# Kernel optimization log

Hardware: AMD Instinct MI355X
Metric: run time of the kernel (lower is better)

Reference implementation:

```python
import jax, jax.numpy as jnp
import numpy as np

N = 30000      # nodes
D = 512        # nhid
E = 300000     # edges (before self-loops)
P_FEAT = 0.5   # feature dropout (F.dropout, training=True)
P_ATT = 0.6    # GATConv attention dropout
NEG_SLOPE = 0.2
SCALE = 1.0    # PairNorm scale


def setup_inputs() -> dict:
    key = jax.random.key(0)
    k1, k2, k3, k4, k5, k6 = jax.random.split(key, 6)
    x = jax.random.normal(k1, (N, D), dtype=jnp.float32)
    edge_index = jax.random.randint(k2, (2, E), 0, N, dtype=jnp.int32)
    # GATConv params (heads=1): lin weight, att_src/att_dst vectors, bias
    W = jax.random.normal(k3, (D, D), dtype=jnp.float32) * 0.05
    att_src = jax.random.normal(k4, (D,), dtype=jnp.float32) * 0.05
    att_dst = jax.random.normal(k5, (D,), dtype=jnp.float32) * 0.05
    bias = jax.random.normal(k6, (D,), dtype=jnp.float32) * 0.05
    return {"x": x, "edge_index": edge_index, "W": W,
            "att_src": att_src, "att_dst": att_dst, "bias": bias}


def reference(x, edge_index, W, att_src, att_dst, bias):
    # deterministic dropout masks (module runs with training=True)
    dk = jax.random.key(42)
    k_feat, k_att = jax.random.split(dk)

    # F.dropout(x, 0.5, training=True)
    keep = jax.random.bernoulli(k_feat, 1.0 - P_FEAT, x.shape)
    x = jnp.where(keep, x / (1.0 - P_FEAT), jnp.float32(0.0))

    # GATConv(heads=1): linear transform
    h = x @ W                                     # [N, D]

    # add self-loops (PyG default add_self_loops=True)
    src, dst = edge_index[0], edge_index[1]
    loop = jnp.arange(N, dtype=src.dtype)
    src = jnp.concatenate([src, loop])            # [E+N]
    dst = jnp.concatenate([dst, loop])

    # per-edge attention logits: LeakyReLU(a_src . h_j + a_dst . h_i)
    a_s = h @ att_src                             # [N]
    a_d = h @ att_dst                             # [N]
    e = jax.nn.leaky_relu(a_s[src] + a_d[dst], NEG_SLOPE)   # [E+N]

    # segment softmax over incoming edges of each dst node
    m = jax.ops.segment_max(e, dst, num_segments=N)
    m = jnp.where(jnp.isfinite(m), m, jnp.float32(0.0))
    ee = jnp.exp(e - m[dst])
    s = jax.ops.segment_sum(ee, dst, num_segments=N)
    alpha = ee / (s[dst] + 1e-16)                 # [E+N]

    # attention dropout p=0.6
    keep_a = jax.random.bernoulli(k_att, 1.0 - P_ATT, alpha.shape)
    alpha = jnp.where(keep_a, alpha / (1.0 - P_ATT), jnp.float32(0.0))

    # scatter-aggregate weighted messages, add bias
    out = jax.ops.segment_sum(alpha[:, None] * h[src], dst, num_segments=N) + bias

    # PairNorm 'PN': center columns, scale by mean row norm
    out = out - jnp.mean(out, axis=0)
    rownorm_mean = jnp.sqrt(1e-6 + jnp.mean(jnp.sum(out * out, axis=1)))
    out = SCALE * out / rownorm_mean

    return jax.nn.relu(out)
```

## Files before the change

kernel.cpp:

```cpp
#include <hip/hip_runtime.h>
#include <stdint.h>
#include <math.h>


#define N_NODES 30000
#define MPAD    30080
#define DIM     512
#define NEDGE   300000
#define ETOT    330000
#define AGG_BLOCKS 7500
#define RED_BLOCKS 60
#define RED_ROWS   125

typedef unsigned int u32;
typedef unsigned short u16;

typedef __attribute__((ext_vector_type(8))) short bf16x8;
typedef __attribute__((ext_vector_type(4))) float f32x4;

__host__ __device__ __forceinline__ void threefry2x32(u32 k0, u32 k1, u32 x0, u32 x1,
                                                      u32& o0, u32& o1) {
  u32 ks2 = k0 ^ k1 ^ 0x1BD11BDAu;
#define TF_R(r) { x0 += x1; x1 = (x1 << r) | (x1 >> (32 - r)); x1 ^= x0; }
  x0 += k0; x1 += k1;
  TF_R(13) TF_R(15) TF_R(26) TF_R(6)
  x0 += k1; x1 += ks2 + 1u;
  TF_R(17) TF_R(29) TF_R(16) TF_R(24)
  x0 += ks2; x1 += k0 + 2u;
  TF_R(13) TF_R(15) TF_R(26) TF_R(6)
  x0 += k0; x1 += k1 + 3u;
  TF_R(17) TF_R(29) TF_R(16) TF_R(24)
  x0 += k1; x1 += ks2 + 4u;
  TF_R(13) TF_R(15) TF_R(26) TF_R(6)
  x0 += ks2; x1 += k0 + 5u;
#undef TF_R
  o0 = x0; o1 = x1;
}

__device__ __forceinline__ u32 tf_fold(u32 k0, u32 k1, u32 idx) {
  u32 a, b;
  threefry2x32(k0, k1, 0u, idx, a, b);
  return a ^ b;
}

__device__ __forceinline__ float bf2f(u32 bits16) {
  return __uint_as_float(bits16 << 16);
}
__device__ __forceinline__ u16 f2bf(float f) {
  u32 u = __float_as_uint(f);
  return (u16)((u + 0x7fffu + ((u >> 16) & 1u)) >> 16);
}

__global__ __launch_bounds__(256) void k_cvtW(const float* __restrict__ W,
                                              u16* __restrict__ Wt) {
  __shared__ u16 tile[32][33];
  int b = blockIdx.x;
  int bk = (b & 15) * 32, bn = (b >> 4) * 32;
  int c = threadIdx.x & 31, r = threadIdx.x >> 5;
#pragma unroll
  for (int rr = 0; rr < 32; rr += 8)
    tile[r + rr][c] = f2bf(W[(size_t)(bk + r + rr) * DIM + bn + c]);
  __syncthreads();
#pragma unroll
  for (int rr = 0; rr < 32; rr += 8)
    Wt[(size_t)(bn + r + rr) * DIM + bk + c] = tile[c][r + rr];
}

__global__ __launch_bounds__(256) void k_dropout(const float* __restrict__ x,
                                                 u16* __restrict__ xd,
                                                 u32 kf0, u32 kf1) {
  size_t gid = (size_t)blockIdx.x * 256 + threadIdx.x;
  size_t i0 = gid * 8;
  if (i0 >= (size_t)MPAD * DIM) return;
  uint4 o = make_uint4(0u, 0u, 0u, 0u);
  if (i0 < (size_t)N_NODES * DIM) {
    float4 v0 = *(const float4*)(x + i0);
    float4 v1 = *(const float4*)(x + i0 + 4);
    float xv[8] = {v0.x, v0.y, v0.z, v0.w, v1.x, v1.y, v1.z, v1.w};
    u32 res[4];
#pragma unroll
    for (int p = 0; p < 4; p++) {
      u32 b0 = tf_fold(kf0, kf1, (u32)i0 + 2 * p);
      u32 b1 = tf_fold(kf0, kf1, (u32)i0 + 2 * p + 1);
      u32 r0 = (b0 >> 31) ? 0u : (u32)f2bf(2.0f * xv[2 * p]);
      u32 r1 = (b1 >> 31) ? 0u : (u32)f2bf(2.0f * xv[2 * p + 1]);
      res[p] = r0 | (r1 << 16);
    }
    o = make_uint4(res[0], res[1], res[2], res[3]);
  }
  *(uint4*)(xd + i0) = o;
}

__global__ __launch_bounds__(256) void k_gemm(const u16* __restrict__ A,
                                              const u16* __restrict__ B,
                                              u16* __restrict__ H) {
  __shared__ __align__(16) u16 lA[128 * 32];
  __shared__ __align__(16) u16 lB[128 * 32];
  const int bn = (blockIdx.x & 3) * 128;
  const int bm = (blockIdx.x >> 2) * 128;
  const int tid = threadIdx.x;
  const int wave = tid >> 6, lane = tid & 63;
  const int quad = lane >> 4, l16 = lane & 15;
  const int wrow = (wave & 1) * 64, wcol = (wave >> 1) * 64;

  f32x4 acc[4][4] = {};
  const int srow = tid >> 2;
  const int scq  = (tid & 3) * 8;

  for (int k0 = 0; k0 < DIM; k0 += 32) {
    uint4 va0 = *(const uint4*)(A + (size_t)(bm + srow) * DIM + k0 + scq);
    uint4 va1 = *(const uint4*)(A + (size_t)(bm + 64 + srow) * DIM + k0 + scq);
    uint4 vb0 = *(const uint4*)(B + (size_t)(bn + srow) * DIM + k0 + scq);
    uint4 vb1 = *(const uint4*)(B + (size_t)(bn + 64 + srow) * DIM + k0 + scq);
    __syncthreads();
    *(uint4*)(lA + srow * 32 + scq) = va0;
    *(uint4*)(lA + (64 + srow) * 32 + scq) = va1;
    *(uint4*)(lB + srow * 32 + scq) = vb0;
    *(uint4*)(lB + (64 + srow) * 32 + scq) = vb1;
    __syncthreads();

    bf16x8 af[4], bfr[4];
#pragma unroll
    for (int i = 0; i < 4; i++)
      af[i] = *(const bf16x8*)(lA + (wrow + i * 16 + l16) * 32 + quad * 8);
#pragma unroll
    for (int j = 0; j < 4; j++)
      bfr[j] = *(const bf16x8*)(lB + (wcol + j * 16 + l16) * 32 + quad * 8);
#pragma unroll
    for (int i = 0; i < 4; i++)
#pragma unroll
      for (int j = 0; j < 4; j++)
        acc[i][j] = __builtin_amdgcn_mfma_f32_16x16x32_bf16(af[i], bfr[j], acc[i][j], 0, 0, 0);
  }
#pragma unroll
  for (int i = 0; i < 4; i++) {
#pragma unroll
    for (int r = 0; r < 4; r++) {
      int row = bm + wrow + i * 16 + quad * 4 + r;
      u16* hp = H + (size_t)row * DIM + bn + wcol + l16;
#pragma unroll
      for (int j = 0; j < 4; j++) hp[j * 16] = f2bf(acc[i][j][r]);
    }
  }
}

__global__ __launch_bounds__(256) void k_rowdots(const u16* __restrict__ h,
                                                 const float* __restrict__ atts,
                                                 const float* __restrict__ attd,
                                                 float* __restrict__ a_s,
                                                 float* __restrict__ a_d) {
  int row = blockIdx.x * 4 + (threadIdx.x >> 6);
  if (row >= N_NODES) return;
  int lane = threadIdx.x & 63;
  uint4 hv = *(const uint4*)(h + (size_t)row * DIM + lane * 8);
  float4 s0 = *(const float4*)(atts + lane * 8);
  float4 s1 = *(const float4*)(atts + lane * 8 + 4);
  float4 d0 = *(const float4*)(attd + lane * 8);
  float4 d1 = *(const float4*)(attd + lane * 8 + 4);
  u32 hw[4] = {hv.x, hv.y, hv.z, hv.w};
  float sa[8] = {s0.x, s0.y, s0.z, s0.w, s1.x, s1.y, s1.z, s1.w};
  float da[8] = {d0.x, d0.y, d0.z, d0.w, d1.x, d1.y, d1.z, d1.w};
  float ps = 0.f, pd = 0.f;
#pragma unroll
  for (int p = 0; p < 4; p++) {
    float h0 = bf2f(hw[p] & 0xffffu), h1 = bf2f(hw[p] >> 16);
    ps += h0 * sa[2 * p] + h1 * sa[2 * p + 1];
    pd += h0 * da[2 * p] + h1 * da[2 * p + 1];
  }
#pragma unroll
  for (int d = 1; d < 64; d <<= 1) { ps += __shfl_xor(ps, d); pd += __shfl_xor(pd, d); }
  if (lane == 0) { a_s[row] = ps; a_d[row] = pd; }
}

__global__ __launch_bounds__(256) void k_hist(const int* __restrict__ ei,
                                              int* __restrict__ counts) {
  int i = blockIdx.x * 256 + threadIdx.x;
  if (i >= ETOT) return;
  int d = (i < NEDGE) ? ei[NEDGE + i] : (i - NEDGE);
  atomicAdd(&counts[d], 1);
}

__global__ __launch_bounds__(1024) void k_scan(const int* __restrict__ counts,
                                               int* __restrict__ off,
                                               int* __restrict__ cursor) {
  __shared__ int wsum[16];
  __shared__ int s_total;
  int tid = threadIdx.x, lane = tid & 63, wid = tid >> 6;
  int carry = 0;
  for (int base = 0; base < N_NODES; base += 1024) {
    int i = base + tid;
    int v = (i < N_NODES) ? counts[i] : 0;
    int x = v;
#pragma unroll
    for (int d = 1; d < 64; d <<= 1) {
      int y = __shfl_up(x, d);
      if (lane >= d) x += y;
    }
    if (lane == 63) wsum[wid] = x;
    __syncthreads();
    if (tid == 0) {
      int run = 0;
#pragma unroll
      for (int w = 0; w < 16; w++) { int tv = wsum[w]; wsum[w] = run; run += tv; }
      s_total = run;
    }
    __syncthreads();
    int excl = x - v + wsum[wid] + carry;
    if (i < N_NODES) { off[i] = excl; cursor[i] = excl; }
    carry += s_total;
    __syncthreads();
  }
  if (tid == 0) off[N_NODES] = carry;
}

__global__ __launch_bounds__(256) void k_scatter(const int* __restrict__ ei,
                                                 int* __restrict__ cursor,
                                                 int* __restrict__ perm) {
  int i = blockIdx.x * 256 + threadIdx.x;
  if (i >= ETOT) return;
  int d = (i < NEDGE) ? ei[NEDGE + i] : (i - NEDGE);
  int slot = atomicAdd(&cursor[d], 1);
  perm[slot] = i;
}

__global__ __launch_bounds__(256) void k_aggregate(
    const int* __restrict__ ei, const int* __restrict__ off, const int* __restrict__ perm,
    const float* __restrict__ a_s, const float* __restrict__ a_d,
    const u16* __restrict__ h, const float* __restrict__ bias,
    float* __restrict__ oa, float* __restrict__ colpart,
    float* __restrict__ ssqpart, u32 ka0, u32 ka1) {
  __shared__ float lbuf[4][512];
  int wid = threadIdx.x >> 6;
  int node = blockIdx.x * 4 + wid;
  int lane = threadIdx.x & 63;
  int beg = off[node], end = off[node + 1];
  int deg = end - beg;
  float adn = a_d[node];

  float acc[8] = {0.f, 0.f, 0.f, 0.f, 0.f, 0.f, 0.f, 0.f};

  if (deg <= 64) {
    int idx = beg + lane;
    bool valid = idx < end;
    int s = 0;
    float lg = -3.0e38f;
    u32 keepbits = 0;
    if (valid) {
      int eid = perm[idx];
      s = (eid < NEDGE) ? ei[eid] : (eid - NEDGE);
      lg = a_s[s] + adn;
      lg = (lg < 0.f) ? 0.2f * lg : lg;
      keepbits = tf_fold(ka0, ka1, (u32)eid);
    }
    float mx = lg;
#pragma unroll
    for (int d = 1; d < 64; d <<= 1) mx = fmaxf(mx, __shfl_xor(mx, d));
    float ee = valid ? expf(lg - mx) : 0.f;
    float ssum = ee;
#pragma unroll
    for (int d = 1; d < 64; d <<= 1) ssum += __shfl_xor(ssum, d);
    float inv_s = 2.5f / (ssum + 1e-16f);
    float w = (valid && ((keepbits >> 9) < 3355444u)) ? ee * inv_s : 0.f;

    for (int j = 0; j < deg; j++) {
      float wj = __shfl(w, j);
      if (wj != 0.f) {
        int sj = __shfl(s, j);
        uint4 hv = *(const uint4*)(h + (size_t)sj * DIM + lane * 8);
        u32 hw[4] = {hv.x, hv.y, hv.z, hv.w};
#pragma unroll
        for (int p = 0; p < 4; p++) {
          acc[2 * p]     += wj * bf2f(hw[p] & 0xffffu);
          acc[2 * p + 1] += wj * bf2f(hw[p] >> 16);
        }
      }
    }
  } else {
    float mx = -3.0e38f;
    for (int base = beg; base < end; base += 64) {
      int idx = base + lane;
      if (idx < end) {
        int eid = perm[idx];
        int s = (eid < NEDGE) ? ei[eid] : (eid - NEDGE);
        float lg = a_s[s] + adn;
        lg = (lg < 0.f) ? 0.2f * lg : lg;
        mx = fmaxf(mx, lg);
      }
    }
#pragma unroll
    for (int d = 1; d < 64; d <<= 1) mx = fmaxf(mx, __shfl_xor(mx, d));
    float ssum = 0.f;
    for (int base = beg; base < end; base += 64) {
      int idx = base + lane;
      if (idx < end) {
        int eid = perm[idx];
        int s = (eid < NEDGE) ? ei[eid] : (eid - NEDGE);
        float lg = a_s[s] + adn;
        lg = (lg < 0.f) ? 0.2f * lg : lg;
        ssum += expf(lg - mx);
      }
    }
#pragma unroll
    for (int d = 1; d < 64; d <<= 1) ssum += __shfl_xor(ssum, d);
    float inv_s = 2.5f / (ssum + 1e-16f);
    for (int base = beg; base < end; base += 64) {
      int idx = base + lane;
      float w = 0.f; int s = 0;
      if (idx < end) {
        int eid = perm[idx];
        s = (eid < NEDGE) ? ei[eid] : (eid - NEDGE);
        float lg = a_s[s] + adn;
        lg = (lg < 0.f) ? 0.2f * lg : lg;
        float ee = expf(lg - mx);
        u32 bits = tf_fold(ka0, ka1, (u32)eid);
        if ((bits >> 9) < 3355444u) w = ee * inv_s;
      }
      int cnt = min(64, end - base);
      for (int j = 0; j < cnt; j++) {
        float wj = __shfl(w, j);
        if (wj != 0.f) {
          int sj = __shfl(s, j);
          uint4 hv = *(const uint4*)(h + (size_t)sj * DIM + lane * 8);
          u32 hw[4] = {hv.x, hv.y, hv.z, hv.w};
#pragma unroll
          for (int p = 0; p < 4; p++) {
            acc[2 * p]     += wj * bf2f(hw[p] & 0xffffu);
            acc[2 * p + 1] += wj * bf2f(hw[p] >> 16);
          }
        }
      }
    }
  }

  float4 b0 = *(const float4*)(bias + lane * 8);
  float4 b1 = *(const float4*)(bias + lane * 8 + 4);
  float bb[8] = {b0.x, b0.y, b0.z, b0.w, b1.x, b1.y, b1.z, b1.w};
  float val[8];
#pragma unroll
  for (int t = 0; t < 8; t++) val[t] = acc[t] + bb[t];
  float* op = oa + (size_t)node * DIM + lane * 8;
#pragma unroll
  for (int t = 0; t < 8; t++) op[t] = val[t];
  *(float4*)&lbuf[wid][lane * 8]     = make_float4(val[0], val[1], val[2], val[3]);
  *(float4*)&lbuf[wid][lane * 8 + 4] = make_float4(val[4], val[5], val[6], val[7]);
  __syncthreads();

  int t = threadIdx.x;
  float s0 = 0.f, s1 = 0.f, ssl = 0.f;
#pragma unroll
  for (int w = 0; w < 4; w++) {
    float a = lbuf[w][t], b = lbuf[w][t + 256];
    s0 += a; s1 += b;
    ssl = fmaf(a, a, ssl);
    ssl = fmaf(b, b, ssl);
  }
  colpart[(size_t)blockIdx.x * 512 + t]       = s0;
  colpart[(size_t)blockIdx.x * 512 + 256 + t] = s1;
#pragma unroll
  for (int d = 1; d < 64; d <<= 1) ssl += __shfl_xor(ssl, d);
  __shared__ float wss[4];
  if ((t & 63) == 0) wss[t >> 6] = ssl;
  __syncthreads();
  if (t == 0) ssqpart[blockIdx.x] = wss[0] + wss[1] + wss[2] + wss[3];
}

__global__ __launch_bounds__(256) void k_redstats(const float* __restrict__ colpart,
                                                  const float* __restrict__ ssqpart,
                                                  float* __restrict__ colsum,
                                                  double* __restrict__ ssq) {
  int b = blockIdx.x;
  int t = threadIdx.x;
  int r0 = b * RED_ROWS;
  float s0 = 0.f, s1 = 0.f;
  for (int r = r0; r < r0 + RED_ROWS; r++) {
    s0 += colpart[(size_t)r * 512 + t];
    s1 += colpart[(size_t)r * 512 + 256 + t];
  }
  atomicAdd(&colsum[t], s0);
  atomicAdd(&colsum[t + 256], s1);
  float sl = (t < RED_ROWS) ? ssqpart[r0 + t] : 0.f;
#pragma unroll
  for (int d = 1; d < 64; d <<= 1) sl += __shfl_xor(sl, d);
  __shared__ float w4[4];
  if ((t & 63) == 0) w4[t >> 6] = sl;
  __syncthreads();
  if (t == 0) atomicAdd(ssq, (double)(w4[0] + w4[1] + w4[2] + w4[3]));
}

__global__ __launch_bounds__(512) void k_finalize(const float* __restrict__ colsum,
                                                  const double* __restrict__ ssq,
                                                  float* __restrict__ mu,
                                                  float* __restrict__ invp) {
  __shared__ double sred[8];
  int j = threadIdx.x;
  float m = colsum[j] * (1.0f / 30000.0f);
  mu[j] = m;
  double p = (double)m * (double)m;
#pragma unroll
  for (int d = 1; d < 64; d <<= 1) p += __shfl_xor(p, d);
  int lane = j & 63, wid = j >> 6;
  if (lane == 0) sred[wid] = p;
  __syncthreads();
  if (j == 0) {
    double smu2 = 0.0;
#pragma unroll
    for (int w = 0; w < 8; w++) smu2 += sred[w];
    double centered = ssq[0] - 30000.0 * smu2;
    double mean = centered * (1.0 / 30000.0);
    if (!(mean >= 0.0)) mean = 0.0;
    float rn = sqrtf(1e-6f + (float)mean);
    invp[0] = 1.0f / rn;
  }
}

__global__ __launch_bounds__(256) void k_finalout(const float* __restrict__ oa,
                                                  const float* __restrict__ mu,
                                                  const float* __restrict__ invp,
                                                  float* __restrict__ out) {
  size_t gid = (size_t)blockIdx.x * 256 + threadIdx.x;
  size_t i0 = gid * 4;
  if (i0 >= (size_t)N_NODES * DIM) return;
  float inv = invp[0];
  int j = (int)(i0 & (DIM - 1));
  float4 v = *(const float4*)(oa + i0);
  float4 m = *(const float4*)(mu + j);
  float4 o;
  o.x = (v.x - m.x) * inv; o.x = (o.x < 0.f) ? 0.f : o.x;
  o.y = (v.y - m.y) * inv; o.y = (o.y < 0.f) ? 0.f : o.y;
  o.z = (v.z - m.z) * inv; o.z = (o.z < 0.f) ? 0.f : o.z;
  o.w = (v.w - m.w) * inv; o.w = (o.w < 0.f) ? 0.f : o.w;
  *(float4*)(out + i0) = o;
}

extern "C" void kernel_launch(void* const* d_in, const int* in_sizes, int n_in,
                              void* d_out, int out_size, void* d_ws, size_t ws_size,
                              hipStream_t stream) {
  const float* x    = (const float*)d_in[0];
  const int*   ei   = (const int*)d_in[1];
  const float* W    = (const float*)d_in[2];
  const float* atts = (const float*)d_in[3];
  const float* attd = (const float*)d_in[4];
  const float* bias = (const float*)d_in[5];
  float* out = (float*)d_out;
  char* ws = (char*)d_ws;

  float* oa     = (float*)(ws + 0);
  u16*   xd     = (u16*)(ws + 0);
  u16*   h      = (u16*)(ws + 61440000);
  u16*   Wt     = (u16*)(ws + 92241920);
  float* a_s    = (float*)(ws + 92766208);
  float* a_d    = (float*)(ws + 92886272);
  int*   counts = (int*)(ws + 93006336);
  int*   offs   = (int*)(ws + 93126400);
  int*   cursor = (int*)(ws + 93246464);
  int*   perm   = (int*)(ws + 93366528);
  float* colsum = (float*)(ws + 94686528);
  float* mu     = (float*)(ws + 94688576);
  double* ssq   = (double*)(ws + 94690624);
  float* invp   = (float*)(ws + 94690688);

  float* colpart = out;
  float* ssqpart = out + (size_t)AGG_BLOCKS * 512;

  u32 kf0, kf1, ka0, ka1;
  threefry2x32(0u, 42u, 0u, 0u, kf0, kf1);
  threefry2x32(0u, 42u, 0u, 1u, ka0, ka1);

  hipMemsetAsync(counts, 0, 120064, stream);
  hipMemsetAsync((void*)colsum, 0, 4224, stream);

  k_cvtW<<<256, 256, 0, stream>>>(W, Wt);
  k_dropout<<<7520, 256, 0, stream>>>(x, xd, kf0, kf1);
  k_gemm<<<940, 256, 0, stream>>>(xd, Wt, h);
  k_rowdots<<<7500, 256, 0, stream>>>(h, atts, attd, a_s, a_d);
  k_hist<<<1290, 256, 0, stream>>>(ei, counts);
  k_scan<<<1, 1024, 0, stream>>>(counts, offs, cursor);
  k_scatter<<<1290, 256, 0, stream>>>(ei, cursor, perm);
  k_aggregate<<<AGG_BLOCKS, 256, 0, stream>>>(ei, offs, perm, a_s, a_d, h, bias,
                                              oa, colpart, ssqpart, ka0, ka1);
  k_redstats<<<RED_BLOCKS, 256, 0, stream>>>(colpart, ssqpart, colsum, ssq);
  k_finalize<<<1, 512, 0, stream>>>(colsum, ssq, mu, invp);
  k_finalout<<<15000, 256, 0, stream>>>(oa, mu, invp, out);
}
```

Measured before the change: 304.3 us.

## Fuse attention row-dots into GEMM epilogue and widen K-tile with padded LDS

Removes the separate rowdots kernel. Each GEMM block now reduces its fp32 accumulators against att_src/att_dst and atomically adds per-row partials into a_s/a_d, which are zeroed by a new memset. The GEMM K-step grows from 32 to 64, and LDS rows are padded to 72 elements to reduce bank conflicts and halve the number of barriers. The changes are a launch removed plus a reread of h avoided, in exchange for float atomics (nondeterministic summation order) and dot products computed on unrounded fp32 values instead of bf16 h.

New measurement: 354.8 us. 1.17x slower.

```diff
diff --git a/kernel.cpp b/kernel.cpp
--- a/kernel.cpp
+++ b/kernel.cpp
@@ -11,6 +11,7 @@
 #define AGG_BLOCKS 7500
 #define RED_BLOCKS 60
 #define RED_ROWS   125
+#define LDSW    72
 
 typedef unsigned int u32;
 typedef unsigned short u16;
@@ -93,9 +94,13 @@
 
 __global__ __launch_bounds__(256) void k_gemm(const u16* __restrict__ A,
                                               const u16* __restrict__ B,
-                                              u16* __restrict__ H) {
-  __shared__ __align__(16) u16 lA[128 * 32];
-  __shared__ __align__(16) u16 lB[128 * 32];
+                                              u16* __restrict__ H,
+                                              const float* __restrict__ atts,
+                                              const float* __restrict__ attd,
+                                              float* __restrict__ a_s,
+                                              float* __restrict__ a_d) {
+  __shared__ __align__(16) u16 lA[128 * LDSW];
+  __shared__ __align__(16) u16 lB[128 * LDSW];
   const int bn = (blockIdx.x & 3) * 128;
   const int bm = (blockIdx.x >> 2) * 128;
   const int tid = threadIdx.x;
@@ -104,34 +109,43 @@
   const int wrow = (wave & 1) * 64, wcol = (wave >> 1) * 64;
 
   f32x4 acc[4][4] = {};
-  const int srow = tid >> 2;
-  const int scq  = (tid & 3) * 8;
-
-  for (int k0 = 0; k0 < DIM; k0 += 32) {
-    uint4 va0 = *(const uint4*)(A + (size_t)(bm + srow) * DIM + k0 + scq);
-    uint4 va1 = *(const uint4*)(A + (size_t)(bm + 64 + srow) * DIM + k0 + scq);
-    uint4 vb0 = *(const uint4*)(B + (size_t)(bn + srow) * DIM + k0 + scq);
-    uint4 vb1 = *(const uint4*)(B + (size_t)(bn + 64 + srow) * DIM + k0 + scq);
+
+  for (int k0 = 0; k0 < DIM; k0 += 64) {
+    uint4 ra[4], rb[4];
+#pragma unroll
+    for (int p = 0; p < 4; p++) {
+      int idx = tid + p * 256;
+      int row = idx >> 3, c8 = idx & 7;
+      ra[p] = *(const uint4*)(A + (size_t)(bm + row) * DIM + k0 + c8 * 8);
+      rb[p] = *(const uint4*)(B + (size_t)(bn + row) * DIM + k0 + c8 * 8);
+    }
     __syncthreads();
-    *(uint4*)(lA + srow * 32 + scq) = va0;
-    *(uint4*)(lA + (64 + srow) * 32 + scq) = va1;
-    *(uint4*)(lB + srow * 32 + scq) = vb0;
-    *(uint4*)(lB + (64 + srow) * 32 + scq) = vb1;
+#pragma unroll
+    for (int p = 0; p < 4; p++) {
+      int idx = tid + p * 256;
+      int row = idx >> 3, c8 = idx & 7;
+      *(uint4*)(lA + row * LDSW + c8 * 8) = ra[p];
+      *(uint4*)(lB + row * LDSW + c8 * 8) = rb[p];
+    }
     __syncthreads();
 
-    bf16x8 af[4], bfr[4];
-#pragma unroll
-    for (int i = 0; i < 4; i++)
-      af[i] = *(const bf16x8*)(lA + (wrow + i * 16 + l16) * 32 + quad * 8);
-#pragma unroll
-    for (int j = 0; j < 4; j++)
-      bfr[j] = *(const bf16x8*)(lB + (wcol + j * 16 + l16) * 32 + quad * 8);
-#pragma unroll
-    for (int i = 0; i < 4; i++)
+#pragma unroll
+    for (int ks = 0; ks < 2; ks++) {
+      bf16x8 af[4], bfr[4];
+#pragma unroll
+      for (int i = 0; i < 4; i++)
+        af[i] = *(const bf16x8*)(lA + (wrow + i * 16 + l16) * LDSW + ks * 32 + quad * 8);
 #pragma unroll
       for (int j = 0; j < 4; j++)
-        acc[i][j] = __builtin_amdgcn_mfma_f32_16x16x32_bf16(af[i], bfr[j], acc[i][j], 0, 0, 0);
-  }
+        bfr[j] = *(const bf16x8*)(lB + (wcol + j * 16 + l16) * LDSW + ks * 32 + quad * 8);
+#pragma unroll
+      for (int i = 0; i < 4; i++)
+#pragma unroll
+        for (int j = 0; j < 4; j++)
+          acc[i][j] = __builtin_amdgcn_mfma_f32_16x16x32_bf16(af[i], bfr[j], acc[i][j], 0, 0, 0);
+    }
+  }
+
 #pragma unroll
   for (int i = 0; i < 4; i++) {
 #pragma unroll
@@ -142,34 +156,34 @@
       for (int j = 0; j < 4; j++) hp[j * 16] = f2bf(acc[i][j][r]);
     }
   }
-}
-
-__global__ __launch_bounds__(256) void k_rowdots(const u16* __restrict__ h,
-                                                 const float* __restrict__ atts,
-                                                 const float* __restrict__ attd,
-                                                 float* __restrict__ a_s,
-                                                 float* __restrict__ a_d) {
-  int row = blockIdx.x * 4 + (threadIdx.x >> 6);
-  if (row >= N_NODES) return;
-  int lane = threadIdx.x & 63;
-  uint4 hv = *(const uint4*)(h + (size_t)row * DIM + lane * 8);
-  float4 s0 = *(const float4*)(atts + lane * 8);
-  float4 s1 = *(const float4*)(atts + lane * 8 + 4);
-  float4 d0 = *(const float4*)(attd + lane * 8);
-  float4 d1 = *(const float4*)(attd + lane * 8 + 4);
-  u32 hw[4] = {hv.x, hv.y, hv.z, hv.w};
-  float sa[8] = {s0.x, s0.y, s0.z, s0.w, s1.x, s1.y, s1.z, s1.w};
-  float da[8] = {d0.x, d0.y, d0.z, d0.w, d1.x, d1.y, d1.z, d1.w};
-  float ps = 0.f, pd = 0.f;
-#pragma unroll
-  for (int p = 0; p < 4; p++) {
-    float h0 = bf2f(hw[p] & 0xffffu), h1 = bf2f(hw[p] >> 16);
-    ps += h0 * sa[2 * p] + h1 * sa[2 * p + 1];
-    pd += h0 * da[2 * p] + h1 * da[2 * p + 1];
-  }
-#pragma unroll
-  for (int d = 1; d < 64; d <<= 1) { ps += __shfl_xor(ps, d); pd += __shfl_xor(pd, d); }
-  if (lane == 0) { a_s[row] = ps; a_d[row] = pd; }
+
+  float as_j[4], ad_j[4];
+#pragma unroll
+  for (int j = 0; j < 4; j++) {
+    int col = bn + wcol + j * 16 + l16;
+    as_j[j] = atts[col];
+    ad_j[j] = attd[col];
+  }
+#pragma unroll
+  for (int i = 0; i < 4; i++) {
+#pragma unroll
+    for (int r = 0; r < 4; r++) {
+      float ps = acc[i][0][r] * as_j[0] + acc[i][1][r] * as_j[1]
+               + acc[i][2][r] * as_j[2] + acc[i][3][r] * as_j[3];
+      float pd = acc[i][0][r] * ad_j[0] + acc[i][1][r] * ad_j[1]
+               + acc[i][2][r] * ad_j[2] + acc[i][3][r] * ad_j[3];
+#pragma unroll
+      for (int d = 1; d < 16; d <<= 1) {
+        ps += __shfl_xor(ps, d);
+        pd += __shfl_xor(pd, d);
+      }
+      int row = bm + wrow + i * 16 + quad * 4 + r;
+      if (l16 == 0 && row < N_NODES) {
+        atomicAdd(&a_s[row], ps);
+        atomicAdd(&a_d[row], pd);
+      }
+    }
+  }
 }
 
 __global__ __launch_bounds__(256) void k_hist(const int* __restrict__ ei,
@@ -468,11 +482,11 @@
 
   hipMemsetAsync(counts, 0, 120064, stream);
   hipMemsetAsync((void*)colsum, 0, 4224, stream);
+  hipMemsetAsync((void*)a_s, 0, 240128, stream);
 
   k_cvtW<<<256, 256, 0, stream>>>(W, Wt);
   k_dropout<<<7520, 256, 0, stream>>>(x, xd, kf0, kf1);
-  k_gemm<<<940, 256, 0, stream>>>(xd, Wt, h);
-  k_rowdots<<<7500, 256, 0, stream>>>(h, atts, attd, a_s, a_d);
+  k_gemm<<<940, 256, 0, stream>>>(xd, Wt, h, atts, attd, a_s, a_d);
   k_hist<<<1290, 256, 0, stream>>>(ei, counts);
   k_scan<<<1, 1024, 0, stream>>>(counts, offs, cursor);
   k_scatter<<<1290, 256, 0, stream>>>(ei, cursor, perm);
```
